# Kernel optimization log

Hardware: AMD Instinct MI355X
Metric: run time of the kernel (lower is better)

## Reference

```python
import jax, jax.numpy as jnp
import numpy as np

DIM = 768
H = 6        # pinned by router mask construction (3 logits -> 6 head gates)
HD = DIM // H  # 128
TAU = 5.0

def setup_inputs() -> dict:
    key = jax.random.key(0)
    ks = jax.random.split(key, 10)
    w = 0.02
    return {
        "x": jax.random.normal(ks[0], (4, 2048, DIM), jnp.float32),
        "latency": jax.random.uniform(ks[1], (1,), jnp.float32),
        "qkv_w": jax.random.normal(ks[2], (3 * DIM, DIM), jnp.float32) * w,
        "qkv_b": jax.random.normal(ks[3], (3 * DIM,), jnp.float32) * w,
        "proj_w": jax.random.normal(ks[4], (DIM, DIM), jnp.float32) * w,
        "proj_b": jax.random.normal(ks[5], (DIM,), jnp.float32) * w,
        "router_w": jax.random.normal(ks[6], (3, 1), jnp.float32),
        "router_b": jax.random.normal(ks[7], (3,), jnp.float32),
        # gumbel noise g = -log(Exp(1)), matching -empty.exponential_().log()
        "g1": -jnp.log(jax.random.exponential(ks[8], (3,), jnp.float32)),
        "g2": -jnp.log(jax.random.exponential(ks[9], (3,), jnp.float32)),
    }

def reference(x, latency, qkv_w, qkv_b, proj_w, proj_b, router_w, router_b, g1, g2):
    # router: Linear(1, 3) on scalar latency -> 3 logits
    logits = router_w @ latency + router_b                      # [3]
    # gumbel-sigmoid, tau=5, hard=True with straight-through estimator
    y_soft = jax.nn.sigmoid((logits + g1 - g2) / TAU)           # [3]
    y_hard = (y_soft > 0.5).astype(y_soft.dtype)
    mask3 = y_hard - jax.lax.stop_gradient(y_soft) + y_soft     # [3]
    # first logit gates 4 heads, remaining two gate one head each -> 6 heads
    mask6 = jnp.concatenate([mask3[:1], mask3[:1], mask3[:1], mask3])  # [6]
    maskC = jnp.repeat(mask6, HD)                               # [DIM]

    B, N, C = x.shape
    qkv = jnp.einsum('bnc,oc->bno', x, qkv_w) + qkv_b           # [B,N,3*DIM]
    qkv = qkv.reshape(B, N, 3, H, HD)
    q, k, v = qkv[:, :, 0], qkv[:, :, 1], qkv[:, :, 2]          # [B,N,H,HD]

    scale = HD ** -0.5
    attn = jax.nn.softmax(jnp.einsum('bqhd,bkhd->bhqk', q * scale, k), axis=-1)
    out = jnp.einsum('bhqk,bkhd->bqhd', attn, v).reshape(B, N, C)

    out = out * maskC                                            # gate heads/channels
    return jnp.einsum('bnc,oc->bno', out, proj_w) + proj_b
```

## Files before the change

### kernel.cpp

```cpp
#include <hip/hip_runtime.h>
#include <cstdint>

#define DIM_ 768
#define H_ 6
#define HD_ 128
#define NB_ 4
#define SEQ_ 2048
#define TOK_ (NB_*SEQ_)
#define OUT3_ (3*DIM_)
#define L2E 1.4426950408889634f

typedef __bf16 bf16;
typedef __bf16 bf16x4 __attribute__((ext_vector_type(4)));
typedef __bf16 bf16x8 __attribute__((ext_vector_type(8)));
typedef float f32x4 __attribute__((ext_vector_type(4)));
typedef float f32x16 __attribute__((ext_vector_type(16)));
typedef unsigned int u32;
typedef u32 u32x4 __attribute__((ext_vector_type(4)));

__device__ __forceinline__ void gload16(const void* g, void* lds) {
  __builtin_amdgcn_global_load_lds((const __attribute__((address_space(1))) void*)g,
                                   (__attribute__((address_space(3))) void*)lds,
                                   16, 0, 0);
}

__global__ void convert_kernel(const float* __restrict__ in, bf16* __restrict__ out, int n) {
  int i = (blockIdx.x * 256 + threadIdx.x) * 4;
  if (i >= n) return;
  float4 v = *reinterpret_cast<const float4*>(in + i);
  bf16x4 o = { (bf16)v.x, (bf16)v.y, (bf16)v.z, (bf16)v.w };
  *reinterpret_cast<bf16x4*>(out + i) = o;
}

__global__ void mask_kernel(const float* __restrict__ latency,
                            const float* __restrict__ rw,
                            const float* __restrict__ rb,
                            const float* __restrict__ g1,
                            const float* __restrict__ g2,
                            float* __restrict__ mask6) {
  int i = threadIdx.x;
  if (i < 6) {
    int j = (i < 4) ? 0 : (i - 3);
    float logit = rw[j] * latency[0] + rb[j];
    float z = (logit + g1[j] - g2[j]) / 5.0f;
    float ys = 1.0f / (1.0f + expf(-z));
    float yh = ys > 0.5f ? 1.0f : 0.0f;
    mask6[i] = (yh - ys) + ys;
  }
}


__global__ __launch_bounds__(256)
void qkv_gemm(const bf16* __restrict__ A, const bf16* __restrict__ W,
              const float* __restrict__ bias,
              bf16* __restrict__ q, bf16* __restrict__ k, bf16* __restrict__ vt) {
  __shared__ bf16 As[128 * 32];
  __shared__ bf16 Bs[128 * 32];
  __shared__ bf16 FragS[8192];
  const int tid = threadIdx.x;
  const int l = tid & 63, w = tid >> 6;
  const int lr = l & 15, lg = l >> 4;
  const int wm = w >> 1, wn = w & 1;
  const int tm = blockIdx.y * 128;
  const int on = blockIdx.x * 128;

  f32x4 acc[4][4];
#pragma unroll
  for (int i = 0; i < 4; ++i)
#pragma unroll
    for (int j = 0; j < 4; ++j) acc[i][j] = f32x4{0.f, 0.f, 0.f, 0.f};

  for (int k0 = 0; k0 < DIM_; k0 += 32) {
    __syncthreads();
#pragma unroll
    for (int u = 0; u < 2; ++u) {
      int row = w * 32 + u * 16 + (l >> 2);
      int cb = l & 3;
      gload16(A + (size_t)(tm + row) * DIM_ + k0 + cb * 8, As + (w * 32 + u * 16) * 32);
      gload16(W + (size_t)(on + row) * DIM_ + k0 + cb * 8, Bs + (w * 32 + u * 16) * 32);
    }
    __syncthreads();
    bf16x8 af[4], bfr[4];
#pragma unroll
    for (int i = 0; i < 4; ++i)
      af[i] = *reinterpret_cast<const bf16x8*>(As + (wm * 64 + i * 16 + lr) * 32 + lg * 8);
#pragma unroll
    for (int j = 0; j < 4; ++j)
      bfr[j] = *reinterpret_cast<const bf16x8*>(Bs + (wn * 64 + j * 16 + lr) * 32 + lg * 8);
#pragma unroll
    for (int i = 0; i < 4; ++i)
#pragma unroll
      for (int j = 0; j < 4; ++j)
        acc[i][j] = __builtin_amdgcn_mfma_f32_16x16x32_bf16(af[i], bfr[j], acc[i][j], 0, 0, 0);
  }

  if (on < 2 * DIM_) {
    const int s = on / DIM_;
    const float scale = 0.08838834764831845f * L2E;
    const int n0 = tm & 2047;
    const int bb = tm >> 11;
    const int hh = (on - s * DIM_) >> 7;
    const int bhh = bb * H_ + hh;
    bf16* dstbase = (s == 0) ? q : k;
    for (int pass = 0; pass < 2; ++pass) {
      __syncthreads();
      if (wm == pass) {
#pragma unroll
        for (int i = 0; i < 4; ++i) {
#pragma unroll
          for (int j = 0; j < 4; ++j) {
            int dd = wn * 64 + j * 16 + lr;
            int kc = dd >> 4, hi8 = (dd >> 3) & 1, e = dd & 7;
            float bia = bias[on + dd];
#pragma unroll
            for (int r = 0; r < 4; ++r) {
              int nl = i * 16 + lg * 4 + r;
              float val = acc[i][j][r] + bia;
              if (s == 0) val *= scale;
              FragS[(((nl >> 5) * 8 + kc) << 9) + ((hi8 * 32 + (nl & 31)) << 3) + e] = (bf16)val;
            }
          }
        }
      }
      __syncthreads();
      size_t base = ((size_t)bhh * 64 + (n0 >> 5) + pass * 2) * 4096;
#pragma unroll
      for (int r8 = 0; r8 < 4; ++r8) {
        bf16x8 v8 = *reinterpret_cast<const bf16x8*>(FragS + r8 * 2048 + tid * 8);
        *reinterpret_cast<bf16x8*>(dstbase + base + r8 * 2048 + tid * 8) = v8;
      }
    }
  } else {
    const int hh = (on - 2 * DIM_) >> 7;
    const int bb = tm >> 11, n0 = tm & 2047;
    const int bhh = bb * H_ + hh;
    bf16(*Ts)[136] = reinterpret_cast<bf16(*)[136]>(As);
    for (int wc = 0; wc < 2; ++wc) {
#pragma unroll
      for (int j = 0; j < 4; ++j) {
        __syncthreads();
        if (wn == wc) {
          float bia = bias[on + wc * 64 + j * 16 + lr];
#pragma unroll
          for (int i = 0; i < 4; ++i) {
            bf16x4 pk;
#pragma unroll
            for (int r = 0; r < 4; ++r) pk[r] = (bf16)(acc[i][j][r] + bia);
            *reinterpret_cast<bf16x4*>(&Ts[lr][wm * 64 + i * 16 + lg * 4]) = pk;
          }
        }
        __syncthreads();
        int row = tid >> 4;
        int c8 = (tid & 15) * 8;
        bf16x8 v8 = *reinterpret_cast<const bf16x8*>(&Ts[row][c8]);
        int d = wc * 64 + j * 16 + row;
        int n = n0 + c8;
        size_t idx = (((((size_t)bhh * 32 + (n >> 6)) * 4 + ((n >> 4) & 3)) * 4 + (d >> 5)) << 9) +
                     ((((n >> 3) & 1) * 32 + (d & 31)) << 3);
        *reinterpret_cast<bf16x8*>(vt + idx) = v8;
      }
    }
  }
}

__global__ __launch_bounds__(256)
void proj_gemm(const bf16* __restrict__ A, const bf16* __restrict__ W,
               const float* __restrict__ bias, float* __restrict__ out) {
  __shared__ bf16 As[128 * 32];
  __shared__ bf16 Bs[128 * 32];
  const int tid = threadIdx.x;
  const int l = tid & 63, w = tid >> 6;
  const int lr = l & 15, lg = l >> 4;
  const int wm = w >> 1, wn = w & 1;
  const int tm = blockIdx.y * 128;
  const int on = blockIdx.x * 128;

  f32x4 acc[4][4];
#pragma unroll
  for (int i = 0; i < 4; ++i)
#pragma unroll
    for (int j = 0; j < 4; ++j) acc[i][j] = f32x4{0.f, 0.f, 0.f, 0.f};

  for (int k0 = 0; k0 < DIM_; k0 += 32) {
    __syncthreads();
#pragma unroll
    for (int u = 0; u < 2; ++u) {
      int row = w * 32 + u * 16 + (l >> 2);
      int cb = l & 3;
      gload16(A + (size_t)(tm + row) * DIM_ + k0 + cb * 8, As + (w * 32 + u * 16) * 32);
      gload16(W + (size_t)(on + row) * DIM_ + k0 + cb * 8, Bs + (w * 32 + u * 16) * 32);
    }
    __syncthreads();
    bf16x8 af[4], bfr[4];
#pragma unroll
    for (int i = 0; i < 4; ++i)
      af[i] = *reinterpret_cast<const bf16x8*>(As + (wm * 64 + i * 16 + lr) * 32 + lg * 8);
#pragma unroll
    for (int j = 0; j < 4; ++j)
      bfr[j] = *reinterpret_cast<const bf16x8*>(Bs + (wn * 64 + j * 16 + lr) * 32 + lg * 8);
#pragma unroll
    for (int i = 0; i < 4; ++i)
#pragma unroll
      for (int j = 0; j < 4; ++j)
        acc[i][j] = __builtin_amdgcn_mfma_f32_16x16x32_bf16(af[i], bfr[j], acc[i][j], 0, 0, 0);
  }

#pragma unroll
  for (int i = 0; i < 4; ++i) {
#pragma unroll
    for (int j = 0; j < 4; ++j) {
      int o = on + wn * 64 + j * 16 + lr;
      float bia = bias[o];
#pragma unroll
      for (int r = 0; r < 4; ++r) {
        int t = tm + wm * 64 + i * 16 + lg * 4 + r;
        out[(size_t)t * DIM_ + o] = acc[i][j][r] + bia;
      }
    }
  }
}

__global__ __launch_bounds__(128)
void attn_kernel(const bf16* __restrict__ qf_g, const bf16* __restrict__ kf_g,
                 const bf16* __restrict__ vf_g, const float* __restrict__ mask6,
                 bf16* __restrict__ ab) {
  __shared__ bf16 KS[3][4096];
  __shared__ bf16 VS[3][4096];

  const int tid = threadIdx.x;
  const int l = tid & 63;
  const int wq = tid >> 6;
  const int kl = l & 31;
  const int hi = l >> 5;
  const int bid = blockIdx.x;
  const int bh = bid % 24;
  const int qt2 = bid / 24;
  const int h = bh % H_;
  const int b = bh / H_;
  const int q0 = qt2 * 64 + wq * 32;
  const int loff = l * 8;
  const float hm = mask6[h];

  if (hm == 0.0f) {
    bf16x8 z = __builtin_bit_cast(bf16x8, u32x4{0u, 0u, 0u, 0u});
    int row = tid >> 1, c0 = (tid & 1) * 64;
    bf16* dst = ab + ((size_t)b * SEQ_ + qt2 * 64 + row) * DIM_ + h * HD_ + c0;
#pragma unroll
    for (int u = 0; u < 8; ++u)
      *reinterpret_cast<bf16x8*>(dst + u * 8) = z;
    return;
  }

  const bf16* qq = qf_g + (((size_t)bh * 64 + qt2 * 2 + wq) * 8) * 512;
  const bf16* kq = kf_g + (size_t)bh * 262144;
  const bf16* vq = vf_g + (size_t)bh * 262144;

  bf16x8 qf[8];
#pragma unroll
  for (int kc = 0; kc < 8; ++kc)
    qf[kc] = *reinterpret_cast<const bf16x8*>(qq + kc * 512 + loff);

  f32x16 oacc[4];
#pragma unroll
  for (int df = 0; df < 4; ++df)
#pragma unroll
    for (int r = 0; r < 16; ++r) oacc[df][r] = 0.f;
  float m_lane = -3.0e38f;
  float lsum = 0.f;

  auto STAGE = [&](int jj, int buf) {
    const bf16* kb = kq + (size_t)jj * 4096;
    const bf16* vb = vq + (size_t)jj * 4096;
#pragma unroll
    for (int u = 0; u < 4; ++u) {
      int c = wq * 4 + u;
      gload16(kb + c * 512 + loff, &KS[buf][c * 512]);
      gload16(vb + c * 512 + loff, &VS[buf][c * 512]);
    }
  };

  STAGE(0, 0);
  STAGE(1, 1);

  for (int jj = 0; jj < 64; ++jj) {
    const int buf = jj % 3;
    asm volatile("s_waitcnt vmcnt(8)" ::: "memory");
    __builtin_amdgcn_s_barrier();
    if (jj + 2 < 64) STAGE(jj + 2, (jj + 2) % 3);

    const bf16* Kc = &KS[buf][0];
    const bf16* Vc = &VS[buf][0];

    f32x16 sacc;
#pragma unroll
    for (int r = 0; r < 16; ++r) sacc[r] = 0.f;
    __builtin_amdgcn_s_setprio(1);
#pragma unroll
    for (int kc = 0; kc < 8; ++kc) {
      bf16x8 kfr = *reinterpret_cast<const bf16x8*>(Kc + kc * 512 + loff);
      sacc = __builtin_amdgcn_mfma_f32_32x32x16_bf16(kfr, qf[kc], sacc, 0, 0, 0);
    }
    __builtin_amdgcn_s_setprio(0);

    float t = sacc[0];
#pragma unroll
    for (int r = 1; r < 16; ++r) t = fmaxf(t, sacc[r]);
    t = fmaxf(t, __shfl_xor(t, 32));
    bool need = t > m_lane + 8.0f;
    if (__ballot(need) != 0ull) {
      float nm = fmaxf(m_lane, t);
      float c = exp2f(m_lane - nm);
      m_lane = nm;
      lsum *= c;
#pragma unroll
      for (int r = 0; r < 16; ++r) {
        float cr = __shfl(c, (r & 3) + 8 * (r >> 2) + 4 * hi);
#pragma unroll
        for (int df = 0; df < 4; ++df) oacc[df][r] *= cr;
      }
    }

    u32 pp[8];
#pragma unroll
    for (int m = 0; m < 8; ++m) {
      float e0 = exp2f(sacc[2 * m] - m_lane);
      float e1 = exp2f(sacc[2 * m + 1] - m_lane);
      lsum += e0 + e1;
      union { u32 u; bf16 hh2[2]; } pk;
      pk.hh2[0] = (bf16)e0; pk.hh2[1] = (bf16)e1;
      pp[m] = pk.u;
    }

    u32x4 afv[2];
#pragma unroll
    for (int ks = 0; ks < 2; ++ks) {
#pragma unroll
      for (int i = 0; i < 2; ++i) {
        u32 a = pp[4 * ks + i];
        u32 b2 = pp[4 * ks + 2 + i];
        asm volatile("v_permlane32_swap_b32 %0, %1" : "+v"(a), "+v"(b2));
        afv[ks][i] = a;
        afv[ks][2 + i] = b2;
      }
    }

    __builtin_amdgcn_s_setprio(1);
#pragma unroll
    for (int ks = 0; ks < 2; ++ks) {
      bf16x8 pa = __builtin_bit_cast(bf16x8, afv[ks]);
#pragma unroll
      for (int df = 0; df < 4; ++df) {
        bf16x8 vfr = *reinterpret_cast<const bf16x8*>(Vc + (ks * 4 + df) * 512 + loff);
        oacc[df] = __builtin_amdgcn_mfma_f32_32x32x16_bf16(pa, vfr, oacc[df], 0, 0, 0);
      }
    }
    __builtin_amdgcn_s_setprio(0);
  }

  float lt = lsum + __shfl_xor(lsum, 32);
  float inv_l = hm / lt;
#pragma unroll
  for (int r = 0; r < 16; ++r) {
    int qloc = (r & 3) + 8 * (r >> 2) + 4 * hi;
    float invr = __shfl(inv_l, qloc);
    int n = q0 + qloc;
#pragma unroll
    for (int df = 0; df < 4; ++df) {
      int d = df * 32 + kl;
      ab[((size_t)b * SEQ_ + n) * DIM_ + h * HD_ + d] = (bf16)(oacc[df][r] * invr);
    }
  }
}

extern "C" void kernel_launch(void* const* d_in, const int* in_sizes, int n_in,
                              void* d_out, int out_size, void* d_ws, size_t ws_size,
                              hipStream_t stream) {
  const float* x        = (const float*)d_in[0];
  const float* latency  = (const float*)d_in[1];
  const float* qkv_w    = (const float*)d_in[2];
  const float* qkv_b    = (const float*)d_in[3];
  const float* proj_w   = (const float*)d_in[4];
  const float* proj_b   = (const float*)d_in[5];
  const float* router_w = (const float*)d_in[6];
  const float* router_b = (const float*)d_in[7];
  const float* g1       = (const float*)d_in[8];
  const float* g2       = (const float*)d_in[9];
  float* out = (float*)d_out;

  const size_t N_X  = (size_t)TOK_ * DIM_;
  const size_t N_WQ = (size_t)OUT3_ * DIM_;
  const size_t N_WP = (size_t)DIM_ * DIM_;
  const size_t N_P  = (size_t)NB_ * H_ * SEQ_ * HD_;

  float* maskp = (float*)d_ws;
  bf16* xb  = (bf16*)((char*)d_ws + 256);
  bf16* wqb = xb + N_X;
  bf16* wpb = wqb + N_WQ;
  bf16* qbf = wpb + N_WP;
  bf16* kbf = qbf + N_P;
  bf16* vtb = kbf + N_P;
  bf16* abf = vtb + N_P;

  size_t need = 256 + 2 * (N_X + N_WQ + N_WP + 4 * N_P);
  if (ws_size < need) return;

  convert_kernel<<<(int)(N_X / 1024), 256, 0, stream>>>(x, xb, (int)N_X);
  convert_kernel<<<(int)(N_WQ / 1024), 256, 0, stream>>>(qkv_w, wqb, (int)N_WQ);
  convert_kernel<<<(int)(N_WP / 1024), 256, 0, stream>>>(proj_w, wpb, (int)N_WP);
  mask_kernel<<<1, 64, 0, stream>>>(latency, router_w, router_b, g1, g2, maskp);

  qkv_gemm<<<dim3(OUT3_ / 128, TOK_ / 128), 256, 0, stream>>>(xb, wqb, qkv_b, qbf, kbf, vtb);
  attn_kernel<<<dim3(24 * (SEQ_ / 64)), 128, 0, stream>>>(qbf, kbf, vtb, maskp, abf);
  proj_gemm<<<dim3(DIM_ / 128, TOK_ / 128), 256, 0, stream>>>(abf, wpb, proj_b, out);
}
```

Before: 206.2 us.

## Skip gated-off heads in GEMMs and widen attention blocks to eight waves

The QKV GEMM now exits early for output tiles belonging to heads whose runtime mask is zero. The projection GEMM skips K-slices of the masked heads, since those attention outputs are zeroed anyway. The mask kernel now runs first so both GEMMs can read it. Separately, the attention kernel goes from 2 to 8 waves per block over 256 queries, so each staged K/V tile is shared by more waves and each thread issues fewer loads. The trade-off is that the grid shrinks to 192 blocks, which may leave compute units idle, and the work skipping only pays off when some heads are actually gated off.

```diff
diff --git a/kernel.cpp b/kernel.cpp
--- a/kernel.cpp
+++ b/kernel.cpp
@@ -52,7 +52,7 @@
 
 __global__ __launch_bounds__(256)
 void qkv_gemm(const bf16* __restrict__ A, const bf16* __restrict__ W,
-              const float* __restrict__ bias,
+              const float* __restrict__ bias, const float* __restrict__ mask6,
               bf16* __restrict__ q, bf16* __restrict__ k, bf16* __restrict__ vt) {
   __shared__ bf16 As[128 * 32];
   __shared__ bf16 Bs[128 * 32];
@@ -64,6 +64,10 @@
   const int tm = blockIdx.y * 128;
   const int on = blockIdx.x * 128;
 
+  const int sblk = (on < DIM_) ? 0 : (on < 2 * DIM_ ? 1 : 2);
+  const int hblk = (on - sblk * DIM_) >> 7;
+  if (mask6[hblk] == 0.0f) return;
+
   f32x4 acc[4][4];
 #pragma unroll
   for (int i = 0; i < 4; ++i)
@@ -95,12 +99,11 @@
   }
 
   if (on < 2 * DIM_) {
-    const int s = on / DIM_;
+    const int s = sblk;
     const float scale = 0.08838834764831845f * L2E;
     const int n0 = tm & 2047;
     const int bb = tm >> 11;
-    const int hh = (on - s * DIM_) >> 7;
-    const int bhh = bb * H_ + hh;
+    const int bhh = bb * H_ + hblk;
     bf16* dstbase = (s == 0) ? q : k;
     for (int pass = 0; pass < 2; ++pass) {
       __syncthreads();
@@ -131,9 +134,8 @@
       }
     }
   } else {
-    const int hh = (on - 2 * DIM_) >> 7;
     const int bb = tm >> 11, n0 = tm & 2047;
-    const int bhh = bb * H_ + hh;
+    const int bhh = bb * H_ + hblk;
     bf16(*Ts)[136] = reinterpret_cast<bf16(*)[136]>(As);
     for (int wc = 0; wc < 2; ++wc) {
 #pragma unroll
@@ -165,7 +167,8 @@
 
 __global__ __launch_bounds__(256)
 void proj_gemm(const bf16* __restrict__ A, const bf16* __restrict__ W,
-               const float* __restrict__ bias, float* __restrict__ out) {
+               const float* __restrict__ bias, const float* __restrict__ mask6,
+               float* __restrict__ out) {
   __shared__ bf16 As[128 * 32];
   __shared__ bf16 Bs[128 * 32];
   const int tid = threadIdx.x;
@@ -182,6 +185,7 @@
     for (int j = 0; j < 4; ++j) acc[i][j] = f32x4{0.f, 0.f, 0.f, 0.f};
 
   for (int k0 = 0; k0 < DIM_; k0 += 32) {
+    if (mask6[k0 >> 7] == 0.0f) continue;
     __syncthreads();
 #pragma unroll
     for (int u = 0; u < 2; ++u) {
@@ -220,7 +224,7 @@
   }
 }
 
-__global__ __launch_bounds__(128)
+__global__ __launch_bounds__(512)
 void attn_kernel(const bf16* __restrict__ qf_g, const bf16* __restrict__ kf_g,
                  const bf16* __restrict__ vf_g, const float* __restrict__ mask6,
                  bf16* __restrict__ ab) {
@@ -229,29 +233,28 @@
 
   const int tid = threadIdx.x;
   const int l = tid & 63;
-  const int wq = tid >> 6;
-  const int kl = l & 31;
-  const int hi = l >> 5;
+  const int w = tid >> 6;
+  const int kl = l & 31, hi = l >> 5;
   const int bid = blockIdx.x;
   const int bh = bid % 24;
-  const int qt2 = bid / 24;
+  const int qg = bid / 24;
   const int h = bh % H_;
   const int b = bh / H_;
-  const int q0 = qt2 * 64 + wq * 32;
+  const int q0 = qg * 256 + w * 32;
   const int loff = l * 8;
   const float hm = mask6[h];
 
   if (hm == 0.0f) {
     bf16x8 z = __builtin_bit_cast(bf16x8, u32x4{0u, 0u, 0u, 0u});
     int row = tid >> 1, c0 = (tid & 1) * 64;
-    bf16* dst = ab + ((size_t)b * SEQ_ + qt2 * 64 + row) * DIM_ + h * HD_ + c0;
+    bf16* dst = ab + ((size_t)b * SEQ_ + qg * 256 + row) * DIM_ + h * HD_ + c0;
 #pragma unroll
     for (int u = 0; u < 8; ++u)
       *reinterpret_cast<bf16x8*>(dst + u * 8) = z;
     return;
   }
 
-  const bf16* qq = qf_g + (((size_t)bh * 64 + qt2 * 2 + wq) * 8) * 512;
+  const bf16* qq = qf_g + (((size_t)bh * 64 + qg * 8 + w) * 8) * 512;
   const bf16* kq = kf_g + (size_t)bh * 262144;
   const bf16* vq = vf_g + (size_t)bh * 262144;
 
@@ -269,14 +272,8 @@
   float lsum = 0.f;
 
   auto STAGE = [&](int jj, int buf) {
-    const bf16* kb = kq + (size_t)jj * 4096;
-    const bf16* vb = vq + (size_t)jj * 4096;
-#pragma unroll
-    for (int u = 0; u < 4; ++u) {
-      int c = wq * 4 + u;
-      gload16(kb + c * 512 + loff, &KS[buf][c * 512]);
-      gload16(vb + c * 512 + loff, &VS[buf][c * 512]);
-    }
+    gload16(kq + (size_t)jj * 4096 + w * 512 + loff, &KS[buf][w * 512]);
+    gload16(vq + (size_t)jj * 4096 + w * 512 + loff, &VS[buf][w * 512]);
   };
 
   STAGE(0, 0);
@@ -284,7 +281,8 @@
 
   for (int jj = 0; jj < 64; ++jj) {
     const int buf = jj % 3;
-    asm volatile("s_waitcnt vmcnt(8)" ::: "memory");
+    if (jj < 62) asm volatile("s_waitcnt vmcnt(2)" ::: "memory");
+    else         asm volatile("s_waitcnt vmcnt(0)" ::: "memory");
     __builtin_amdgcn_s_barrier();
     if (jj + 2 < 64) STAGE(jj + 2, (jj + 2) % 3);
 
@@ -404,12 +402,12 @@
   size_t need = 256 + 2 * (N_X + N_WQ + N_WP + 4 * N_P);
   if (ws_size < need) return;
 
+  mask_kernel<<<1, 64, 0, stream>>>(latency, router_w, router_b, g1, g2, maskp);
   convert_kernel<<<(int)(N_X / 1024), 256, 0, stream>>>(x, xb, (int)N_X);
   convert_kernel<<<(int)(N_WQ / 1024), 256, 0, stream>>>(qkv_w, wqb, (int)N_WQ);
   convert_kernel<<<(int)(N_WP / 1024), 256, 0, stream>>>(proj_w, wpb, (int)N_WP);
-  mask_kernel<<<1, 64, 0, stream>>>(latency, router_w, router_b, g1, g2, maskp);
-
-  qkv_gemm<<<dim3(OUT3_ / 128, TOK_ / 128), 256, 0, stream>>>(xb, wqb, qkv_b, qbf, kbf, vtb);
-  attn_kernel<<<dim3(24 * (SEQ_ / 64)), 128, 0, stream>>>(qbf, kbf, vtb, maskp, abf);
-  proj_gemm<<<dim3(DIM_ / 128, TOK_ / 128), 256, 0, stream>>>(abf, wpb, proj_b, out);
-}
+
+  qkv_gemm<<<dim3(OUT3_ / 128, TOK_ / 128), 256, 0, stream>>>(xb, wqb, qkv_b, maskp, qbf, kbf, vtb);
+  attn_kernel<<<dim3(24 * 8), 512, 0, stream>>>(qbf, kbf, vtb, maskp, abf);
+  proj_gemm<<<dim3(DIM_ / 128, TOK_ / 128), 256, 0, stream>>>(abf, wpb, proj_b, maskp, out);
+}
```

New measurement: 201.9 us. 1.02x faster.
